# Kernel tuning notes

Measured on AMD Instinct MI355X. Metric: run time of the kernel, lower is better.

Reference implementation:

```python
import jax, jax.numpy as jnp
import numpy as np

B, T_AUDIO, T_TEXT, D = 16, 4096, 1024, 512


def setup_inputs() -> dict:
    key = jax.random.key(0)
    k1, k2, k3, k4, k5 = jax.random.split(key, 5)
    audio_feats = jax.random.normal(k1, (B, T_AUDIO, D), dtype=jnp.float32)
    audio_feats_len = jnp.full((B,), T_AUDIO, dtype=jnp.int32)
    text_token_for_audio = jax.random.randint(k2, (B, T_TEXT), 0, 32000, dtype=jnp.int32)
    text_token_embed_for_audio = jax.random.normal(k3, (B, T_TEXT, D), dtype=jnp.float32) * 0.02
    text_token_len = jax.random.randint(k4, (B,), 1, T_TEXT + 1, dtype=jnp.int32)
    # start/end frame indices per token; sort last axis so start <= end
    asr_alignment = jnp.sort(jax.random.randint(k5, (B, T_TEXT, 2), 0, T_AUDIO, dtype=jnp.int32), axis=-1)
    return {
        'audio_feats': audio_feats,
        'audio_feats_len': audio_feats_len,
        'text_token_for_audio': text_token_for_audio,
        'text_token_embed_for_audio': text_token_embed_for_audio,
        'text_token_len': text_token_len,
        'asr_alignment': asr_alignment,
    }


def reference(audio_feats, audio_feats_len, text_token_for_audio,
              text_token_embed_for_audio, text_token_len, asr_alignment):
    Bv, Ta, Dv = audio_feats.shape
    Tt = text_token_for_audio.shape[1]
    idx = jnp.arange(Ta, dtype=asr_alignment.dtype)  # [Ta]
    # ~make_pad_mask: True where token position is valid
    token_mask = jnp.arange(Tt)[None, :] < text_token_len[:, None]          # [B,Tt]
    span_mask = (idx[None, None, :] >= asr_alignment[:, :, 0:1]) & \
                (idx[None, None, :] <= asr_alignment[:, :, 1:2])            # [B,Tt,Ta]
    mask = (token_mask[:, :, None] & span_mask).astype(audio_feats.dtype)  # [B,Tt,Ta]
    # masked sum over audio frames, then divide by counts (0/0 -> 0, matching nan_to_num)
    sums = jnp.einsum('bta,bad->btd', mask, audio_feats)                    # [B,Tt,D]
    counts = jnp.sum(mask, axis=-1, keepdims=True)                          # [B,Tt,1]
    segmented_feats = jnp.where(counts > 0, sums / jnp.where(counts > 0, counts, 1.0), 0.0)
    return segmented_feats, text_token_len
```

## Files before the change

### kernel.cpp

```cpp
#include <hip/hip_runtime.h>


constexpr int Bv  = 16;
constexpr int TA  = 4096;
constexpr int TT  = 1024;
constexpr int Dv  = 512;
constexpr int D4  = Dv / 4;
constexpr int CH  = 16;
constexpr int NCk = TA / CH;
constexpr int NC1 = NCk + 1;
constexpr int NSL = 7;

typedef float    f32x4 __attribute__((ext_vector_type(4)));
typedef _Float16 f16x4 __attribute__((ext_vector_type(4)));

__device__ __forceinline__ void f4add(float4& a, const float4& v) {
    a.x += v.x; a.y += v.y; a.z += v.z; a.w += v.w;
}
__device__ __forceinline__ void f4addh(float4& a, const f16x4& v) {
    a.x += (float)v.x; a.y += (float)v.y; a.z += (float)v.z; a.w += (float)v.w;
}
__device__ __forceinline__ f16x4 toh4(const float4& v) {
    f16x4 r = { (_Float16)v.x, (_Float16)v.y, (_Float16)v.z, (_Float16)v.w };
    return r;
}

__global__ __launch_bounds__(256) void k_partials(
    const float4* __restrict__ A, f16x4* __restrict__ P, f16x4* __restrict__ S)
{
    int g  = blockIdx.x * 256 + threadIdx.x;
    int d4 = g & (D4 - 1);
    int c  = (g >> 7) & (NCk - 1);
    int b  = g >> 15;
    size_t abase = (size_t)(b * TA + c * CH) * D4 + d4;
    size_t pbase = ((size_t)(b * NCk + c) * NSL) * D4 + d4;
    float4 acc = {0.f, 0.f, 0.f, 0.f};
    #pragma unroll
    for (int i = 0; i < CH; ++i) {
        float4 v = A[abase + (size_t)i * D4];
        f4add(acc, v);
        if ((i & 1) && i < 15)
            P[pbase + (size_t)((i - 1) >> 1) * D4] = toh4(acc);
    }
    S[(size_t)(b * NCk + c) * D4 + d4] = toh4(acc);
}

__global__ __launch_bounds__(64) void k_scan(
    const f16x4* __restrict__ S, float4* __restrict__ C,
    const int* __restrict__ tlen, float* __restrict__ outt)
{
    __shared__ float4 lds[16][4];
    int tid = threadIdx.x;
    int col = tid & 3;
    int g   = tid >> 2;
    int b   = blockIdx.x >> 5;
    int d4  = (blockIdx.x & 31) * 4 + col;

    float4 run = {0.f, 0.f, 0.f, 0.f};
    float4 excl[16];
    #pragma unroll
    for (int i = 0; i < 16; ++i) {
        excl[i] = run;
        f4addh(run, S[(size_t)(b * NCk + g * 16 + i) * D4 + d4]);
    }
    lds[g][col] = run;
    __syncthreads();
    float4 go = {0.f, 0.f, 0.f, 0.f};
    for (int gp = 0; gp < g; ++gp)
        f4add(go, lds[gp][col]);

    size_t cb = (size_t)b * NC1 * D4 + d4;
    #pragma unroll
    for (int i = 0; i < 16; ++i) {
        float4 cex = go;
        f4add(cex, excl[i]);
        C[cb + (size_t)(g * 16 + i) * D4] = cex;
    }
    if (g == 15) {
        float4 tot = go;
        f4add(tot, run);
        C[cb + (size_t)NCk * D4] = tot;
    }
    if (blockIdx.x == 0 && tid < Bv)
        outt[tid] = (float)tlen[tid];
}

__global__ __launch_bounds__(128) void k_tokens(
    const float4* __restrict__ A, const f16x4* __restrict__ P,
    const float4* __restrict__ C, const int* __restrict__ tlen,
    const int* __restrict__ align, float4* __restrict__ out)
{
    int xcd  = blockIdx.x & 7;
    int slot = blockIdx.x >> 3;
    int b  = xcd + 8 * (slot >> 10);
    int t  = slot & (TT - 1);
    int bt = b * TT + t;
    int d4 = threadIdx.x;
    size_t ob = (size_t)bt * D4 + d4;

    if (t >= tlen[b]) {
        f32x4 z = {0.f, 0.f, 0.f, 0.f};
        __builtin_nontemporal_store(z, (f32x4*)&out[ob]);
        return;
    }
    int s = align[2 * bt];
    int e = align[2 * bt + 1];

    const float4* Ab = A + (size_t)b * TA * D4;
    const float4* Cb = C + (size_t)b * NC1 * D4;
    const f16x4*  Pb = P + (size_t)b * NCk * NSL * D4;

    auto Eval = [&](int x) -> float4 {
        int c  = x >> 4;
        int k2 = (x & 15) >> 1;
        float4 v = Cb[(size_t)c * D4 + d4];
        if (k2) f4addh(v, Pb[((size_t)c * NSL + (k2 - 1)) * D4 + d4]);
        if (x & 1) f4add(v, Ab[(size_t)(x - 1) * D4 + d4]);
        return v;
    };

    float4 hi = Eval(e + 1);
    float4 lo = Eval(s);
    float inv = 1.f / (float)(e - s + 1);
    f32x4 r = { (hi.x - lo.x) * inv, (hi.y - lo.y) * inv,
                (hi.z - lo.z) * inv, (hi.w - lo.w) * inv };
    __builtin_nontemporal_store(r, (f32x4*)&out[ob]);
}

extern "C" void kernel_launch(void* const* d_in, const int* in_sizes, int n_in,
                              void* d_out, int out_size, void* d_ws, size_t ws_size,
                              hipStream_t stream)
{
    const float* audio = (const float*)d_in[0];
    const int*   tlen  = (const int*)d_in[4];
    const int*   align = (const int*)d_in[5];
    float* out = (float*)d_out;

    f16x4*  P = (f16x4*)d_ws;
    f16x4*  S = P + (size_t)Bv * NCk * NSL * D4;
    float4* C = (float4*)(S + (size_t)Bv * NCk * D4);

    k_partials<<<(Bv * NCk * D4) / 256, 256, 0, stream>>>(
        (const float4*)audio, P, S);
    k_scan<<<Bv * 32, 64, 0, stream>>>(
        S, C, tlen, out + (size_t)Bv * TT * Dv);
    k_tokens<<<Bv * TT, 128, 0, stream>>>(
        (const float4*)audio, P, C, tlen, align, (float4*)out);
}
```

Before: 45.32 us.

## Fuse partials, scan and token phases into one cooperative persistent kernel

Merges the three launches (chunk partial sums, per-batch scan, per-token span means) into one persistent cooperative kernel that separates the phases with grid-wide syncs. The aim is to remove inter-kernel launch gaps and tail drain. The scan phase is restructured to 256-thread units covering 16 columns, and token work now packs two tokens per 256-thread block. The change risks grid.sync overhead, reduced parallelism from capping the grid at occupancy, and extra host-side attribute queries on every call. The original three-kernel path is kept as a fallback.

```diff
diff --git a/kernel.cpp b/kernel.cpp
--- a/kernel.cpp
+++ b/kernel.cpp
@@ -1,4 +1,7 @@
 #include <hip/hip_runtime.h>
+#include <hip/hip_cooperative_groups.h>
+
+namespace cg = cooperative_groups;
 
 
 constexpr int Bv  = 16;
@@ -10,6 +13,11 @@
 constexpr int NCk = TA / CH;
 constexpr int NC1 = NCk + 1;
 constexpr int NSL = 7;
+constexpr int NTHR = 256;
+
+constexpr int AUNITS = (Bv * NCk * D4) / NTHR;
+constexpr int BUNITS = 128;
+constexpr int CUNITS = 8192;
 
 typedef float    f32x4 __attribute__((ext_vector_type(4)));
 typedef _Float16 f16x4 __attribute__((ext_vector_type(4)));
@@ -25,10 +33,12 @@
     return r;
 }
 
-__global__ __launch_bounds__(256) void k_partials(
-    const float4* __restrict__ A, f16x4* __restrict__ P, f16x4* __restrict__ S)
-{
-    int g  = blockIdx.x * 256 + threadIdx.x;
+
+__device__ __forceinline__ void phaseA_unit(
+    int u, int tid, const float4* __restrict__ A,
+    f16x4* __restrict__ P, f16x4* __restrict__ S)
+{
+    int g  = u * NTHR + tid;
     int d4 = g & (D4 - 1);
     int c  = (g >> 7) & (NCk - 1);
     int b  = g >> 15;
@@ -45,6 +55,115 @@
     S[(size_t)(b * NCk + c) * D4 + d4] = toh4(acc);
 }
 
+__device__ __forceinline__ void phaseC_unit(
+    int v, int tid, const float4* __restrict__ A, const f16x4* __restrict__ P,
+    const float4* __restrict__ C, const int* __restrict__ tlen,
+    const int* __restrict__ align, float4* __restrict__ out)
+{
+    int xcd  = v & 7;
+    int w    = v >> 3;
+    int half = tid >> 7;
+    int d4   = tid & 127;
+    int slot = w * 2 + half;
+    int b  = xcd + 8 * (slot >> 10);
+    int t  = slot & (TT - 1);
+    int bt = b * TT + t;
+    size_t ob = (size_t)bt * D4 + d4;
+
+    if (t >= tlen[b]) {
+        f32x4 z = {0.f, 0.f, 0.f, 0.f};
+        __builtin_nontemporal_store(z, (f32x4*)&out[ob]);
+        return;
+    }
+    int s = align[2 * bt];
+    int e = align[2 * bt + 1];
+
+    const float4* Ab = A + (size_t)b * TA * D4;
+    const float4* Cb = C + (size_t)b * NC1 * D4;
+    const f16x4*  Pb = P + (size_t)b * NCk * NSL * D4;
+
+    auto Eval = [&](int x) -> float4 {
+        int c  = x >> 4;
+        int k2 = (x & 15) >> 1;
+        float4 vv = Cb[(size_t)c * D4 + d4];
+        if (k2) f4addh(vv, Pb[((size_t)c * NSL + (k2 - 1)) * D4 + d4]);
+        if (x & 1) f4add(vv, Ab[(size_t)(x - 1) * D4 + d4]);
+        return vv;
+    };
+
+    float4 hi = Eval(e + 1);
+    float4 lo = Eval(s);
+    float inv = 1.f / (float)(e - s + 1);
+    f32x4 r = { (hi.x - lo.x) * inv, (hi.y - lo.y) * inv,
+                (hi.z - lo.z) * inv, (hi.w - lo.w) * inv };
+    __builtin_nontemporal_store(r, (f32x4*)&out[ob]);
+}
+
+
+__global__ __launch_bounds__(NTHR, 2) void k_fused(
+    const float4* __restrict__ A, f16x4* __restrict__ P, f16x4* __restrict__ S,
+    float4* __restrict__ C, const int* __restrict__ tlen,
+    const int* __restrict__ align, float4* __restrict__ out,
+    float* __restrict__ outt)
+{
+    cg::grid_group grid = cg::this_grid();
+    int tid = threadIdx.x;
+    __shared__ float4 lds[16][16];
+
+    for (int u = blockIdx.x; u < AUNITS; u += gridDim.x)
+        phaseA_unit(u, tid, A, P, S);
+
+    grid.sync();
+
+    for (int u = blockIdx.x; u < BUNITS; u += gridDim.x) {
+        int j  = tid & 15;
+        int g  = tid >> 4;
+        int b  = u >> 3;
+        int d4 = (u & 7) * 16 + j;
+
+        float4 run = {0.f, 0.f, 0.f, 0.f};
+        float4 excl[16];
+        #pragma unroll
+        for (int i = 0; i < 16; ++i) {
+            excl[i] = run;
+            f4addh(run, S[(size_t)(b * NCk + g * 16 + i) * D4 + d4]);
+        }
+        lds[g][j] = run;
+        __syncthreads();
+        float4 go = {0.f, 0.f, 0.f, 0.f};
+        for (int gp = 0; gp < g; ++gp)
+            f4add(go, lds[gp][j]);
+
+        size_t cb = (size_t)b * NC1 * D4 + d4;
+        #pragma unroll
+        for (int i = 0; i < 16; ++i) {
+            float4 cex = go;
+            f4add(cex, excl[i]);
+            C[cb + (size_t)(g * 16 + i) * D4] = cex;
+        }
+        if (g == 15) {
+            float4 tot = go;
+            f4add(tot, run);
+            C[cb + (size_t)NCk * D4] = tot;
+        }
+        if (u == 0 && tid < Bv)
+            outt[tid] = (float)tlen[tid];
+        __syncthreads();
+    }
+
+    grid.sync();
+
+    for (int v = blockIdx.x; v < CUNITS; v += gridDim.x)
+        phaseC_unit(v, tid, A, P, C, tlen, align, out);
+}
+
+
+__global__ __launch_bounds__(256) void k_partials(
+    const float4* __restrict__ A, f16x4* __restrict__ P, f16x4* __restrict__ S)
+{
+    phaseA_unit(blockIdx.x, threadIdx.x, A, P, S);
+}
+
 __global__ __launch_bounds__(64) void k_scan(
     const f16x4* __restrict__ S, float4* __restrict__ C,
     const int* __restrict__ tlen, float* __restrict__ outt)
@@ -85,65 +204,55 @@
         outt[tid] = (float)tlen[tid];
 }
 
-__global__ __launch_bounds__(128) void k_tokens(
+__global__ __launch_bounds__(256) void k_tokens(
     const float4* __restrict__ A, const f16x4* __restrict__ P,
     const float4* __restrict__ C, const int* __restrict__ tlen,
     const int* __restrict__ align, float4* __restrict__ out)
 {
-    int xcd  = blockIdx.x & 7;
-    int slot = blockIdx.x >> 3;
-    int b  = xcd + 8 * (slot >> 10);
-    int t  = slot & (TT - 1);
-    int bt = b * TT + t;
-    int d4 = threadIdx.x;
-    size_t ob = (size_t)bt * D4 + d4;
-
-    if (t >= tlen[b]) {
-        f32x4 z = {0.f, 0.f, 0.f, 0.f};
-        __builtin_nontemporal_store(z, (f32x4*)&out[ob]);
-        return;
-    }
-    int s = align[2 * bt];
-    int e = align[2 * bt + 1];
-
-    const float4* Ab = A + (size_t)b * TA * D4;
-    const float4* Cb = C + (size_t)b * NC1 * D4;
-    const f16x4*  Pb = P + (size_t)b * NCk * NSL * D4;
-
-    auto Eval = [&](int x) -> float4 {
-        int c  = x >> 4;
-        int k2 = (x & 15) >> 1;
-        float4 v = Cb[(size_t)c * D4 + d4];
-        if (k2) f4addh(v, Pb[((size_t)c * NSL + (k2 - 1)) * D4 + d4]);
-        if (x & 1) f4add(v, Ab[(size_t)(x - 1) * D4 + d4]);
-        return v;
-    };
-
-    float4 hi = Eval(e + 1);
-    float4 lo = Eval(s);
-    float inv = 1.f / (float)(e - s + 1);
-    f32x4 r = { (hi.x - lo.x) * inv, (hi.y - lo.y) * inv,
-                (hi.z - lo.z) * inv, (hi.w - lo.w) * inv };
-    __builtin_nontemporal_store(r, (f32x4*)&out[ob]);
+    phaseC_unit(blockIdx.x, threadIdx.x, A, P, C, tlen, align, out);
 }
 
 extern "C" void kernel_launch(void* const* d_in, const int* in_sizes, int n_in,
                               void* d_out, int out_size, void* d_ws, size_t ws_size,
                               hipStream_t stream)
 {
-    const float* audio = (const float*)d_in[0];
-    const int*   tlen  = (const int*)d_in[4];
-    const int*   align = (const int*)d_in[5];
-    float* out = (float*)d_out;
+    const float4* audio = (const float4*)d_in[0];
+    const int*    tlen  = (const int*)d_in[4];
+    const int*    align = (const int*)d_in[5];
+    float4* out  = (float4*)d_out;
+    float*  outt = (float*)d_out + (size_t)Bv * TT * Dv;
 
     f16x4*  P = (f16x4*)d_ws;
     f16x4*  S = P + (size_t)Bv * NCk * NSL * D4;
     float4* C = (float4*)(S + (size_t)Bv * NCk * D4);
 
-    k_partials<<<(Bv * NCk * D4) / 256, 256, 0, stream>>>(
-        (const float4*)audio, P, S);
-    k_scan<<<Bv * 32, 64, 0, stream>>>(
-        S, C, tlen, out + (size_t)Bv * TT * Dv);
-    k_tokens<<<Bv * TT, 128, 0, stream>>>(
-        (const float4*)audio, P, C, tlen, align, (float4*)out);
-}
+    bool launched = false;
+    int dev = 0;
+    if (hipGetDevice(&dev) == hipSuccess) {
+        int coop = 0, cus = 0, perCU = 0;
+        (void)hipDeviceGetAttribute(&coop, hipDeviceAttributeCooperativeLaunch, dev);
+        (void)hipDeviceGetAttribute(&cus, hipDeviceAttributeMultiprocessorCount, dev);
+        if (coop && cus > 0 &&
+            hipOccupancyMaxActiveBlocksPerMultiprocessor(
+                &perCU, (const void*)k_fused, NTHR, 0) == hipSuccess &&
+            perCU > 0) {
+            long cap = (long)perCU * cus;
+            int nblk = (int)(cap > 1024 ? 1024 : cap);
+            nblk &= ~7;
+            if (nblk >= 128) {
+                void* args[] = { (void*)&audio, (void*)&P, (void*)&S, (void*)&C,
+                                 (void*)&tlen, (void*)&align, (void*)&out,
+                                 (void*)&outt };
+                launched = (hipLaunchCooperativeKernel(
+                                (const void*)k_fused, dim3(nblk), dim3(NTHR),
+                                args, 0, stream) == hipSuccess);
+            }
+        }
+    }
+
+    if (!launched) {
+        k_partials<<<AUNITS, NTHR, 0, stream>>>(audio, P, S);
+        k_scan<<<Bv * 32, 64, 0, stream>>>(S, C, tlen, outt);
+        k_tokens<<<CUNITS, NTHR, 0, stream>>>(audio, P, C, tlen, align, out);
+    }
+}
```

After: 178.2 us. +293.2%, slower.
